# Performance work log

Hardware: AMD Instinct MI355X
Metric: run time of the kernel (lower is better)

The kernel has to match this reference:

```python
import math
import jax, jax.numpy as jnp
import numpy as np

D_, H_, W_ = 8, 7, 7
N_ = D_ * H_ * W_          # 392 tokens per window
C_ = 128                   # dim
NH, NP = 8, 4              # heads, sampling points
HD = C_ // NH              # head dim 16
PI = math.pi


def _layernorm(x, g, b, eps=1e-5):
    mu = jnp.mean(x, -1, keepdims=True)
    var = jnp.mean((x - mu) ** 2, -1, keepdims=True)
    return (x - mu) * jax.lax.rsqrt(var + eps) * g + b


def _reference_points():
    # torch.meshgrid default 'ij' indexing; linspace(0.5, S-0.5, S)/S
    rz = (jnp.arange(D_, dtype=jnp.float32) + 0.5) / D_
    ry = (jnp.arange(H_, dtype=jnp.float32) + 0.5) / H_
    rx = (jnp.arange(W_, dtype=jnp.float32) + 0.5) / W_
    z, y, x = jnp.meshgrid(rz, ry, rx, indexing='ij')
    # stacked (x, y, z), flattened in (D,H,W) order -> (N, 3)
    return jnp.stack([x.reshape(-1), y.reshape(-1), z.reshape(-1)], -1)


def _trilinear_sample(grid, loc):
    """grid: (B, D, H, W, nh, hd); loc: (B, N, nh, P, 3) normalized [0,1] xyz.
    grid_sample-style: align_corners=False, zero padding."""
    B = grid.shape[0]
    px = loc[..., 0] * W_ - 0.5
    py = loc[..., 1] * H_ - 0.5
    pz = loc[..., 2] * D_ - 0.5
    x0 = jnp.floor(px); y0 = jnp.floor(py); z0 = jnp.floor(pz)
    wx = px - x0; wy = py - y0; wz = pz - z0
    x0i = x0.astype(jnp.int32); y0i = y0.astype(jnp.int32); z0i = z0.astype(jnp.int32)
    b = jnp.arange(B)[:, None, None, None]
    h = jnp.arange(NH)[None, None, :, None]
    out = jnp.zeros(loc.shape[:-1] + (HD,), grid.dtype)
    for dz in (0, 1):
        for dy in (0, 1):
            for dx in (0, 1):
                xi = x0i + dx; yi = y0i + dy; zi = z0i + dz
                w = ((wx if dx else 1.0 - wx) * (wy if dy else 1.0 - wy)
                     * (wz if dz else 1.0 - wz))
                valid = ((xi >= 0) & (xi < W_) & (yi >= 0) & (yi < H_)
                         & (zi >= 0) & (zi < D_))
                v = grid[b, jnp.clip(zi, 0, D_ - 1), jnp.clip(yi, 0, H_ - 1),
                         jnp.clip(xi, 0, W_ - 1), h]          # (B,N,nh,P,hd)
                out = out + (w * valid.astype(w.dtype))[..., None] * v
    return out


def _forward(x, mask, w_value, b_value, w_off, b_off, w_attn, b_attn,
             w_out, b_out, w_proj, b_proj, ln_g, ln_b):
    Bt, N, C = x.shape          # (nW*B, N, C)
    nW = mask.shape[0]
    # --- PositionEmbeddingSine ---
    z_e = jnp.cumsum(mask, 2) * mask / PI
    y_e = jnp.cumsum(mask, 3) * mask / PI
    x_e = jnp.cumsum(mask, 4) * mask / PI
    embed = mask * (jnp.sin(x_e) + jnp.sin(PI * y_e) + z_e)
    matrix_embed = embed.reshape(nW, N, -1)                 # (nW, N, N)
    diag = jnp.diagonal(matrix_embed, axis1=1, axis2=2)     # (nW, N)
    # --- with_pos_embed ---
    q = (x.reshape(-1, nW, N, C) + diag[None, :, :, None]).reshape(x.shape)
    # --- MS3DDeformAttn (single level, Deformable-DETR style, 3D) ---
    ref = _reference_points()                               # (N, 3)
    value = (x @ w_value + b_value).reshape(Bt, D_, H_, W_, NH, HD)
    off = (q @ w_off + b_off).reshape(Bt, N, NH, NP, 3)
    aw = jax.nn.softmax((q @ w_attn + b_attn).reshape(Bt, N, NH, NP), axis=-1)
    normalizer = jnp.array([W_, H_, D_], jnp.float32)
    loc = ref[None, :, None, None, :] + off / normalizer    # (Bt,N,nh,P,3)
    sampled = _trilinear_sample(value, loc)                 # (Bt,N,nh,P,hd)
    attn = (sampled * aw[..., None]).sum(3).reshape(Bt, N, C) @ w_out + b_out
    # --- residual LN + proj ---
    return _layernorm(x + attn, ln_g, ln_b) @ w_proj + b_proj


def setup_inputs() -> dict:
    key = jax.random.key(0)
    ks = jax.random.split(key, 8)
    Bt = 256
    x = jax.random.normal(ks[0], (Bt, N_, C_), jnp.float32)
    mask = jnp.ones((Bt, N_, D_, H_, W_), jnp.float32)

    def lin(k, fi, fo):
        kw, kb = jax.random.split(k)
        s = 1.0 / np.sqrt(fi)
        return (jax.random.uniform(kw, (fi, fo), jnp.float32, -s, s),
                jax.random.uniform(kb, (fo,), jnp.float32, -s, s))

    w_value, b_value = lin(ks[1], C_, C_)
    w_off, b_off = lin(ks[2], C_, NH * NP * 3)
    w_attn, b_attn = lin(ks[3], C_, NH * NP)
    w_out, b_out = lin(ks[4], C_, C_)
    w_proj, b_proj = lin(ks[5], C_, C_)
    return {"x": x, "mask": mask, "w_value": w_value, "b_value": b_value,
            "w_off": w_off, "b_off": b_off, "w_attn": w_attn, "b_attn": b_attn,
            "w_out": w_out, "b_out": b_out, "w_proj": w_proj, "b_proj": b_proj,
            "ln_g": jnp.ones((C_,), jnp.float32),
            "ln_b": jnp.zeros((C_,), jnp.float32)}


def reference(x, mask, w_value, b_value, w_off, b_off, w_attn, b_attn,
              w_out, b_out, w_proj, b_proj, ln_g, ln_b):
    return _forward(x, mask, w_value, b_value, w_off, b_off, w_attn, b_attn,
                    w_out, b_out, w_proj, b_proj, ln_g, ln_b)
```

## Files before the change

kernel.cpp:

```cpp
#include <hip/hip_runtime.h>
#include <hip/hip_fp16.h>

#define NTOK 392
#define NC 128
#define VNC (NTOK * NC)
#define STRIPS 25
#define PI_F 3.14159265358979323846f

typedef __bf16 bf16_t;
typedef bf16_t bf16x8 __attribute__((ext_vector_type(8)));
typedef unsigned short u16;
typedef u16 u16x8 __attribute__((ext_vector_type(8)));
typedef float f32x4 __attribute__((ext_vector_type(4)));

union Frag { u16x8 u; bf16x8 b; };

__device__ __forceinline__ u16 f2bf(float f) {
    unsigned u = __float_as_uint(f);
    unsigned r = (u + 0x7FFFu + ((u >> 16) & 1u)) >> 16;
    return (u16)r;
}
__device__ __forceinline__ float bf2f(u16 u) {
    return __uint_as_float(((unsigned)u) << 16);
}

__global__ void prep_kernel(const float* __restrict__ w_value,
                            const float* __restrict__ w_off,
                            const float* __restrict__ w_attn,
                            const float* __restrict__ w_out,
                            const float* __restrict__ w_proj,
                            u16* __restrict__ wfrag,
                            float* __restrict__ colsum) {
    int g = blockIdx.x * 256 + threadIdx.x;
    if (g < 8192) {
        int lane = g & 63;
        int ks = (g >> 6) & 3;
        int nt = (g >> 8) & 7;
        int set = g >> 11;
        int col = nt * 16 + (lane & 15);
        int k0 = ks * 32 + ((lane >> 4) << 3);
#pragma unroll
        for (int i = 0; i < 8; i++) {
            int k = k0 + i;
            float v;
            if (set == 0)      v = w_value[k * 128 + col];
            else if (set == 1) v = (col < 96) ? w_off[k * 96 + col] : w_attn[k * 32 + col - 96];
            else if (set == 2) v = w_out[k * 128 + col];
            else               v = w_proj[k * 128 + col];
            wfrag[(size_t)g * 8 + i] = f2bf(v);
        }
    } else if (g < 8192 + 128) {
        int o = g - 8192;
        float s = 0.f;
        for (int c2 = 0; c2 < 128; c2++)
            s += (o < 96) ? w_off[c2 * 96 + o] : w_attn[c2 * 32 + o - 96];
        colsum[o] = s;
    }
}

__device__ __forceinline__ void gemm8(const Frag* A, const u16* __restrict__ wf,
                                      int set, int lane, f32x4* C) {
#pragma unroll
    for (int nt = 0; nt < 8; nt++) {
        f32x4 acc = {0.f, 0.f, 0.f, 0.f};
#pragma unroll
        for (int ks = 0; ks < 4; ks++) {
            Frag B;
            B.u = *(const u16x8*)(wf + ((size_t)(((set * 8 + nt) * 4 + ks) * 64 + lane)) * 8);
            acc = __builtin_amdgcn_mfma_f32_16x16x32_bf16(A[ks].b, B.b, acc, 0, 0, 0);
        }
        C[nt] = acc;
    }
}

__device__ __forceinline__ u16x8 pack8(float4 a, float4 b) {
    u16x8 r;
    r[0] = f2bf(a.x); r[1] = f2bf(a.y); r[2] = f2bf(a.z); r[3] = f2bf(a.w);
    r[4] = f2bf(b.x); r[5] = f2bf(b.y); r[6] = f2bf(b.z); r[7] = f2bf(b.w);
    return r;
}

__device__ __forceinline__ void decode_bid(int bid, int& w, int& g) {
    int xcd = bid & 7;
    int q = bid >> 3;
    g = q % 7;
    w = ((q / 7) << 3) | xcd;
}

__global__ __launch_bounds__(256, 4) void value_kernel(
    const float* __restrict__ x, const float* __restrict__ mask,
    const u16* __restrict__ wfrag, const float* __restrict__ b_value,
    u16* __restrict__ value_ws, float* __restrict__ diag_ws) {
    int w, g;
    decode_bid(blockIdx.x, w, g);
    int lane = threadIdx.x & 63;
    int wv = threadIdx.x >> 6;
    int s = g * 4 + wv;
    if (s >= STRIPS) return;
    int t0 = s * 16;
    const float* xb = x + (size_t)w * VNC;

    if (lane < 16) {
        int n = t0 + lane;
        if (n < NTOK) {
            int d = n / 49; int rr = n - d * 49; int h = rr / 7; int ww = rr - h * 7;
            const float* mb = mask + ((size_t)w * NTOK + n) * NTOK;
            float sz = 0.f, sy = 0.f, sx = 0.f;
#pragma unroll
            for (int k = 0; k < 8; k++) { float v = mb[k * 49 + h * 7 + ww]; sz += (k <= d) ? v : 0.f; }
#pragma unroll
            for (int k = 0; k < 7; k++) { float v = mb[d * 49 + k * 7 + ww]; sy += (k <= h) ? v : 0.f; }
#pragma unroll
            for (int k = 0; k < 7; k++) { float v = mb[d * 49 + h * 7 + k]; sx += (k <= ww) ? v : 0.f; }
            float m = mb[d * 49 + h * 7 + ww];
            float xe = sx * m / PI_F, ye = sy * m / PI_F, ze = sz * m / PI_F;
            diag_ws[w * NTOK + n] = m * (sinf(xe) + sinf(PI_F * ye) + ze);
        }
    }

    int arow = t0 + (lane & 15); if (arow > NTOK - 1) arow = NTOK - 1;
    Frag A[4];
#pragma unroll
    for (int ks = 0; ks < 4; ks++) {
        const float4* p = (const float4*)(xb + (size_t)arow * NC + ks * 32 + ((lane >> 4) << 3));
        A[ks].u = pack8(p[0], p[1]);
    }
    f32x4 C[8];
    gemm8(A, wfrag, 0, lane, C);
    u16* vb = value_ws + (size_t)w * VNC;
#pragma unroll
    for (int nt = 0; nt < 8; nt++) {
        int col = nt * 16 + (lane & 15);
        float bv = b_value[col];
#pragma unroll
        for (int reg = 0; reg < 4; reg++) {
            int r = t0 + ((lane >> 4) << 2) + reg;
            if (r < NTOK) vb[r * NC + col] = f2bf(C[nt][reg] + bv);
        }
    }
}

__global__ __launch_bounds__(256, 6) void attn_kernel(
    const float* __restrict__ x, const u16* __restrict__ wfrag,
    const float* __restrict__ colsum_ws, const u16* __restrict__ value_ws,
    const float* __restrict__ diag_ws,
    const float* __restrict__ b_off, const float* __restrict__ b_attn,
    const float* __restrict__ b_out, const float* __restrict__ b_proj,
    const float* __restrict__ ln_g, const float* __restrict__ ln_b,
    float* __restrict__ out) {
    __shared__ __align__(16) u16 scr[4][2048];
    __shared__ float colsum_lds[128], bias2_lds[128], bout_lds[128];
    __shared__ float lng_lds[128], lnb_lds[128], bproj_lds[128];

    int w, g;
    decode_bid(blockIdx.x, w, g);
    int tid = threadIdx.x;
    int lane = tid & 63;
    int wv = tid >> 6;

    if (tid < 128) {
        colsum_lds[tid] = colsum_ws[tid];
        bias2_lds[tid] = (tid < 96) ? b_off[tid] : b_attn[tid - 96];
        bout_lds[tid] = b_out[tid];
        lng_lds[tid] = ln_g[tid];
        lnb_lds[tid] = ln_b[tid];
        bproj_lds[tid] = b_proj[tid];
    }
    __syncthreads();

    int s = g * 4 + wv;
    if (s >= STRIPS) return;
    int t0 = s * 16;
    const float* xb = x + (size_t)w * VNC;
    const u16* vb = value_ws + (size_t)w * VNC;
    float* outb = out + (size_t)w * VNC;

    int arow = t0 + (lane & 15); if (arow > NTOK - 1) arow = NTOK - 1;
    Frag A1[4];
#pragma unroll
    for (int ks = 0; ks < 4; ks++) {
        const float4* p = (const float4*)(xb + (size_t)arow * NC + ks * 32 + ((lane >> 4) << 3));
        A1[ks].u = pack8(p[0], p[1]);
    }
    f32x4 C1[8];
    gemm8(A1, wfrag, 1, lane, C1);

#pragma unroll
    for (int nt = 0; nt < 8; nt++) {
        int col = nt * 16 + (lane & 15);
        float cs = colsum_lds[col];
        float b2 = bias2_lds[col];
#pragma unroll
        for (int reg = 0; reg < 4; reg++) {
            int r = ((lane >> 4) << 2) + reg;
            int gt = t0 + r;
            float dg = diag_ws[w * NTOK + (gt < NTOK ? gt : NTOK - 1)];
            float v = C1[nt][reg] + dg * cs + b2;
            if (nt < 6) {
                scr[wv][r * 96 + col] = __half_as_ushort(__float2half(v));
            } else {
                float m = fmaxf(v, __shfl_xor(v, 1));
                m = fmaxf(m, __shfl_xor(m, 2));
                float e = expf(v - m);
                float s2 = e + __shfl_xor(e, 1);
                s2 += __shfl_xor(s2, 2);
                scr[wv][1536 + r * 32 + (col - 96)] =
                    __half_as_ushort(__float2half(e / s2));
            }
        }
    }

    float acc[2][16];
#pragma unroll
    for (int j = 0; j < 2; j++)
#pragma unroll
        for (int e = 0; e < 16; e++) acc[j][e] = 0.f;

#pragma unroll
    for (int j = 0; j < 2; j++) {
        int t = j * 8 + (lane >> 3);
        int hh = lane & 7;
        int gt = t0 + t;
        int gtc = gt < NTOK ? gt : NTOK - 1;
        int dd = gtc / 49; int rr = gtc - dd * 49;
        int hy = rr / 7;   int wq = rr - hy * 7;
#pragma unroll
        for (int p = 0; p < 4; p++) {
            int ob = t * 96 + (hh * 4 + p) * 3;
            float ox = __half2float(__ushort_as_half(scr[wv][ob + 0]));
            float oy = __half2float(__ushort_as_half(scr[wv][ob + 1]));
            float oz = __half2float(__ushort_as_half(scr[wv][ob + 2]));
            float aw = __half2float(__ushort_as_half(scr[wv][1536 + t * 32 + hh * 4 + p]));
            float px = (float)wq + ox;
            float py = (float)hy + oy;
            float pz = (float)dd + oz;
            float fx = floorf(px), fy = floorf(py), fz = floorf(pz);
            float wxf = px - fx, wyf = py - fy, wzf = pz - fz;
            int ix = (int)fx, iy = (int)fy, iz = (int)fz;
#pragma unroll
            for (int c = 0; c < 8; c++) {
                int dx = c & 1, dy = (c >> 1) & 1, dz = c >> 2;
                int xi = ix + dx, yi = iy + dy, zi = iz + dz;
                if (xi < 0 || xi >= 7 || yi < 0 || yi >= 7 || zi < 0 || zi >= 8) continue;
                float wgt = (dx ? wxf : 1.f - wxf) * (dy ? wyf : 1.f - wyf)
                          * (dz ? wzf : 1.f - wzf) * aw;
                const u16x8* vp = (const u16x8*)(vb + (zi * 49 + yi * 7 + xi) * NC + hh * 16);
                u16x8 v0 = vp[0], v1 = vp[1];
#pragma unroll
                for (int e = 0; e < 8; e++) {
                    acc[j][e]     += wgt * bf2f(v0[e]);
                    acc[j][8 + e] += wgt * bf2f(v1[e]);
                }
            }
        }
    }

#pragma unroll
    for (int j = 0; j < 2; j++) {
        int t = j * 8 + (lane >> 3);
        int hh = lane & 7;
        int sw = (t & 7) << 3;
        u16x8 o0, o1;
#pragma unroll
        for (int e = 0; e < 8; e++) { o0[e] = f2bf(acc[j][e]); o1[e] = f2bf(acc[j][8 + e]); }
        *(u16x8*)&scr[wv][t * NC + ((hh * 16) ^ sw)] = o0;
        *(u16x8*)&scr[wv][t * NC + ((hh * 16 + 8) ^ sw)] = o1;
    }

    Frag A2[4];
#pragma unroll
    for (int ks = 0; ks < 4; ks++) {
        int rowt = lane & 15;
        int c0 = ks * 32 + ((lane >> 4) << 3);
        A2[ks].u = *(const u16x8*)&scr[wv][rowt * NC + (c0 ^ ((rowt & 7) << 3))];
    }
    f32x4 C2[8];
    gemm8(A2, wfrag, 2, lane, C2);

#pragma unroll
    for (int reg = 0; reg < 4; reg++) {
        int r = ((lane >> 4) << 2) + reg;
        int gt = t0 + r;
        int gtc = gt < NTOK ? gt : NTOK - 1;
        float vrow[8];
        float sm = 0.f, sq = 0.f;
#pragma unroll
        for (int nt = 0; nt < 8; nt++) {
            int col = nt * 16 + (lane & 15);
            float v = C2[nt][reg] + bout_lds[col] + xb[(size_t)gtc * NC + col];
            vrow[nt] = v; sm += v; sq += v * v;
        }
        sm += __shfl_xor(sm, 1); sm += __shfl_xor(sm, 2);
        sm += __shfl_xor(sm, 4); sm += __shfl_xor(sm, 8);
        sq += __shfl_xor(sq, 1); sq += __shfl_xor(sq, 2);
        sq += __shfl_xor(sq, 4); sq += __shfl_xor(sq, 8);
        float mu = sm * (1.f / 128.f);
        float var = sq * (1.f / 128.f) - mu * mu;
        float rs = rsqrtf(var + 1e-5f);
#pragma unroll
        for (int nt = 0; nt < 8; nt++) {
            int col = nt * 16 + (lane & 15);
            float xn = (vrow[nt] - mu) * rs * lng_lds[col] + lnb_lds[col];
            scr[wv][r * NC + (col ^ ((r & 7) << 3))] = f2bf(xn);
        }
    }

    Frag A3[4];
#pragma unroll
    for (int ks = 0; ks < 4; ks++) {
        int rowt = lane & 15;
        int c0 = ks * 32 + ((lane >> 4) << 3);
        A3[ks].u = *(const u16x8*)&scr[wv][rowt * NC + (c0 ^ ((rowt & 7) << 3))];
    }
    f32x4 C3[8];
    gemm8(A3, wfrag, 3, lane, C3);
#pragma unroll
    for (int nt = 0; nt < 8; nt++) {
        int col = nt * 16 + (lane & 15);
        float bp = bproj_lds[col];
#pragma unroll
        for (int reg = 0; reg < 4; reg++) {
            int gt = t0 + ((lane >> 4) << 2) + reg;
            if (gt < NTOK) outb[(size_t)gt * NC + col] = C3[nt][reg] + bp;
        }
    }
}

extern "C" void kernel_launch(void* const* d_in, const int* in_sizes, int n_in,
                              void* d_out, int out_size, void* d_ws, size_t ws_size,
                              hipStream_t stream) {
    const float* x       = (const float*)d_in[0];
    const float* mask    = (const float*)d_in[1];
    const float* w_value = (const float*)d_in[2];
    const float* b_value = (const float*)d_in[3];
    const float* w_off   = (const float*)d_in[4];
    const float* b_off   = (const float*)d_in[5];
    const float* w_attn  = (const float*)d_in[6];
    const float* b_attn  = (const float*)d_in[7];
    const float* w_out   = (const float*)d_in[8];
    const float* b_out   = (const float*)d_in[9];
    const float* w_proj  = (const float*)d_in[10];
    const float* b_proj  = (const float*)d_in[11];
    const float* ln_g    = (const float*)d_in[12];
    const float* ln_b    = (const float*)d_in[13];
    float* out = (float*)d_out;

    u16* wfrag     = (u16*)d_ws;
    float* colsum  = (float*)((char*)d_ws + 131072);
    float* diag_ws = (float*)((char*)d_ws + 131584);
    u16* value_ws  = (u16*)((char*)d_ws + 532992);

    prep_kernel<<<33, 256, 0, stream>>>(w_value, w_off, w_attn, w_out, w_proj,
                                        wfrag, colsum);

    int Bt = in_sizes[0] / VNC;
    int nblk = Bt * 7;
    value_kernel<<<nblk, 256, 0, stream>>>(x, mask, wfrag, b_value,
                                           value_ws, diag_ws);
    attn_kernel<<<nblk, 256, 0, stream>>>(x, wfrag, colsum, value_ws, diag_ws,
                                          b_off, b_attn, b_out, b_proj,
                                          ln_g, ln_b, out);
}
```

Before: 179.2 us.

## Interleave offset/attention columns per point, vectorize LDS reads and packed FMA sampling

```diff
diff --git a/kernel.cpp b/kernel.cpp
--- a/kernel.cpp
+++ b/kernel.cpp
@@ -11,9 +11,12 @@
 typedef bf16_t bf16x8 __attribute__((ext_vector_type(8)));
 typedef unsigned short u16;
 typedef u16 u16x8 __attribute__((ext_vector_type(8)));
+typedef u16 u16x4 __attribute__((ext_vector_type(4)));
 typedef float f32x4 __attribute__((ext_vector_type(4)));
+typedef float f32x2 __attribute__((ext_vector_type(2)));
 
 union Frag { u16x8 u; bf16x8 b; };
+union V16 { u16x8 u; unsigned w[4]; };
 
 __device__ __forceinline__ u16 f2bf(float f) {
     unsigned u = __float_as_uint(f);
@@ -44,16 +47,22 @@
             int k = k0 + i;
             float v;
             if (set == 0)      v = w_value[k * 128 + col];
-            else if (set == 1) v = (col < 96) ? w_off[k * 96 + col] : w_attn[k * 32 + col - 96];
+            else if (set == 1) {
+                int h = col >> 4, p = (col >> 2) & 3, e = col & 3;
+                v = (e < 3) ? w_off[k * 96 + (h * 4 + p) * 3 + e]
+                            : w_attn[k * 32 + h * 4 + p];
+            }
             else if (set == 2) v = w_out[k * 128 + col];
             else               v = w_proj[k * 128 + col];
             wfrag[(size_t)g * 8 + i] = f2bf(v);
         }
     } else if (g < 8192 + 128) {
         int o = g - 8192;
+        int h = o >> 4, p = (o >> 2) & 3, e = o & 3;
         float s = 0.f;
         for (int c2 = 0; c2 < 128; c2++)
-            s += (o < 96) ? w_off[c2 * 96 + o] : w_attn[c2 * 32 + o - 96];
+            s += (e < 3) ? w_off[c2 * 96 + (h * 4 + p) * 3 + e]
+                         : w_attn[c2 * 32 + h * 4 + p];
         colsum[o] = s;
     }
 }
@@ -140,7 +149,7 @@
     }
 }
 
-__global__ __launch_bounds__(256, 6) void attn_kernel(
+__global__ __launch_bounds__(256, 4) void attn_kernel(
     const float* __restrict__ x, const u16* __restrict__ wfrag,
     const float* __restrict__ colsum_ws, const u16* __restrict__ value_ws,
     const float* __restrict__ diag_ws,
@@ -159,8 +168,9 @@
     int wv = tid >> 6;
 
     if (tid < 128) {
+        int h = tid >> 4, p = (tid >> 2) & 3, e = tid & 3;
         colsum_lds[tid] = colsum_ws[tid];
-        bias2_lds[tid] = (tid < 96) ? b_off[tid] : b_attn[tid - 96];
+        bias2_lds[tid] = (e < 3) ? b_off[(h * 4 + p) * 3 + e] : b_attn[h * 4 + p];
         bout_lds[tid] = b_out[tid];
         lng_lds[tid] = ln_g[tid];
         lnb_lds[tid] = ln_b[tid];
@@ -185,6 +195,13 @@
     f32x4 C1[8];
     gemm8(A1, wfrag, 1, lane, C1);
 
+    float dg4[4];
+#pragma unroll
+    for (int reg = 0; reg < 4; reg++) {
+        int gt = t0 + ((lane >> 4) << 2) + reg;
+        dg4[reg] = diag_ws[w * NTOK + (gt < NTOK ? gt : NTOK - 1)];
+    }
+
 #pragma unroll
     for (int nt = 0; nt < 8; nt++) {
         int col = nt * 16 + (lane & 15);
@@ -193,28 +210,22 @@
 #pragma unroll
         for (int reg = 0; reg < 4; reg++) {
             int r = ((lane >> 4) << 2) + reg;
-            int gt = t0 + r;
-            float dg = diag_ws[w * NTOK + (gt < NTOK ? gt : NTOK - 1)];
-            float v = C1[nt][reg] + dg * cs + b2;
-            if (nt < 6) {
-                scr[wv][r * 96 + col] = __half_as_ushort(__float2half(v));
-            } else {
-                float m = fmaxf(v, __shfl_xor(v, 1));
-                m = fmaxf(m, __shfl_xor(m, 2));
-                float e = expf(v - m);
-                float s2 = e + __shfl_xor(e, 1);
-                s2 += __shfl_xor(s2, 2);
-                scr[wv][1536 + r * 32 + (col - 96)] =
-                    __half_as_ushort(__float2half(e / s2));
-            }
-        }
-    }
-
-    float acc[2][16];
+            float v = C1[nt][reg] + dg4[reg] * cs + b2;
+            float ex = __expf(v);
+            float s2 = ex + __shfl_xor(ex, 4);
+            s2 += __shfl_xor(s2, 8);
+            float awv = ex * __builtin_amdgcn_rcpf(s2);
+            float outv = ((lane & 3) == 3) ? awv : v;
+            scr[wv][(r * 128 + col) ^ ((r & 3) << 2)] =
+                __half_as_ushort(__float2half(outv));
+        }
+    }
+
+    f32x2 acc2[2][8];
 #pragma unroll
     for (int j = 0; j < 2; j++)
 #pragma unroll
-        for (int e = 0; e < 16; e++) acc[j][e] = 0.f;
+        for (int k = 0; k < 8; k++) acc2[j][k] = (f32x2){0.f, 0.f};
 
 #pragma unroll
     for (int j = 0; j < 2; j++) {
@@ -226,11 +237,12 @@
         int hy = rr / 7;   int wq = rr - hy * 7;
 #pragma unroll
         for (int p = 0; p < 4; p++) {
-            int ob = t * 96 + (hh * 4 + p) * 3;
-            float ox = __half2float(__ushort_as_half(scr[wv][ob + 0]));
-            float oy = __half2float(__ushort_as_half(scr[wv][ob + 1]));
-            float oz = __half2float(__ushort_as_half(scr[wv][ob + 2]));
-            float aw = __half2float(__ushort_as_half(scr[wv][1536 + t * 32 + hh * 4 + p]));
+            int ei = (t * 128 + hh * 16 + p * 4) ^ ((t & 3) << 2);
+            u16x4 q4 = *(const u16x4*)&scr[wv][ei];
+            float ox = __half2float(__ushort_as_half(q4[0]));
+            float oy = __half2float(__ushort_as_half(q4[1]));
+            float oz = __half2float(__ushort_as_half(q4[2]));
+            float aw = __half2float(__ushort_as_half(q4[3]));
             float px = (float)wq + ox;
             float py = (float)hy + oy;
             float pz = (float)dd + oz;
@@ -244,12 +256,18 @@
                 if (xi < 0 || xi >= 7 || yi < 0 || yi >= 7 || zi < 0 || zi >= 8) continue;
                 float wgt = (dx ? wxf : 1.f - wxf) * (dy ? wyf : 1.f - wyf)
                           * (dz ? wzf : 1.f - wzf) * aw;
-                const u16x8* vp = (const u16x8*)(vb + (zi * 49 + yi * 7 + xi) * NC + hh * 16);
-                u16x8 v0 = vp[0], v1 = vp[1];
-#pragma unroll
-                for (int e = 0; e < 8; e++) {
-                    acc[j][e]     += wgt * bf2f(v0[e]);
-                    acc[j][8 + e] += wgt * bf2f(v1[e]);
+                const V16* vp = (const V16*)(vb + (zi * 49 + yi * 7 + xi) * NC + hh * 16);
+                V16 v0 = vp[0], v1 = vp[1];
+                f32x2 wcf = {wgt, wgt};
+#pragma unroll
+                for (int k = 0; k < 4; k++) {
+                    f32x2 a, b;
+                    a.x = __uint_as_float(v0.w[k] << 16);
+                    a.y = __uint_as_float(v0.w[k] & 0xffff0000u);
+                    b.x = __uint_as_float(v1.w[k] << 16);
+                    b.y = __uint_as_float(v1.w[k] & 0xffff0000u);
+                    acc2[j][k]     += wcf * a;
+                    acc2[j][4 + k] += wcf * b;
                 }
             }
         }
@@ -262,7 +280,12 @@
         int sw = (t & 7) << 3;
         u16x8 o0, o1;
 #pragma unroll
-        for (int e = 0; e < 8; e++) { o0[e] = f2bf(acc[j][e]); o1[e] = f2bf(acc[j][8 + e]); }
+        for (int k = 0; k < 4; k++) {
+            o0[2 * k]     = f2bf(acc2[j][k].x);
+            o0[2 * k + 1] = f2bf(acc2[j][k].y);
+            o1[2 * k]     = f2bf(acc2[j][4 + k].x);
+            o1[2 * k + 1] = f2bf(acc2[j][4 + k].y);
+        }
         *(u16x8*)&scr[wv][t * NC + ((hh * 16) ^ sw)] = o0;
         *(u16x8*)&scr[wv][t * NC + ((hh * 16 + 8) ^ sw)] = o1;
     }
```

New measurement: 153.2 us. 1.17x faster.
